# Kernel tuning notes

Hardware: AMD Instinct MI355X
Metric: run time of the kernel (lower is better)

## Reference

```python
import jax, jax.numpy as jnp
import numpy as np

N_HEAD = 16

def setup_inputs() -> dict:
    key = jax.random.key(0)
    k1, k2, k3, k4 = jax.random.split(key, 4)
    B, S, D = 4, 1024, 1024
    x = jax.random.normal(k1, (B, S, D), dtype=jnp.float32)
    # 0/1 float mask: cls_mask[:,0] overrides row 0, cls_mask[:,1] overrides col 0
    cls_mask = jax.random.randint(k2, (B, 2, S), 0, 2).astype(jnp.float32)
    w_attn = jax.random.normal(k3, (D, 3 * D), dtype=jnp.float32) * 0.02
    b_attn = jnp.zeros((3 * D,), dtype=jnp.float32)
    w_proj = jax.random.normal(k4, (D, D), dtype=jnp.float32) * 0.02
    b_proj = jnp.zeros((D,), dtype=jnp.float32)
    return {"x": x, "cls_mask": cls_mask, "w_attn": w_attn, "b_attn": b_attn,
            "w_proj": w_proj, "b_proj": b_proj}

def reference(x, cls_mask, w_attn, b_attn, w_proj, b_proj):
    B, S, D = x.shape
    H = N_HEAD
    hd = D // H
    cm = jnp.broadcast_to(jnp.tril(jnp.ones((S, S), x.dtype))[None, None], (B, 1, S, S))
    cm = cm.at[:, :, 0, :].set(cls_mask[:, 0][:, None, :])
    cm = cm.at[:, :, :, 0].set(cls_mask[:, 1][:, None, :])
    qkv = x @ w_attn + b_attn                      # [B,S,3D]
    q, k, v = jnp.split(qkv, 3, axis=-1)
    split_heads = lambda t: t.reshape(B, S, H, hd).transpose(0, 2, 1, 3)  # [B,H,S,hd]
    q, k, v = split_heads(q), split_heads(k), split_heads(v)
    w = jnp.einsum('bhqd,bhkd->bhqk', q, k) / jnp.sqrt(jnp.asarray(hd, x.dtype))
    w = w * cm - 10000.0 * (1.0 - cm)
    w = jax.nn.softmax(w, axis=-1)
    a = jnp.einsum('bhqk,bhkd->bhqd', w, v)
    a = a.transpose(0, 2, 1, 3).reshape(B, S, D)   # merge heads
    a = a @ w_proj + b_proj
    present = jnp.stack((k, v))                    # [2,B,H,S,hd]
    return a, present
```

## Files before the change

### kernel.cpp

```cpp
#include <hip/hip_runtime.h>
#include <hip/hip_bf16.h>

typedef __bf16 bf16x8 __attribute__((ext_vector_type(8)));
typedef float f32x4 __attribute__((ext_vector_type(4)));

__device__ __forceinline__ f32x4 mfma16(bf16x8 a, bf16x8 b, f32x4 c) {
    return __builtin_amdgcn_mfma_f32_16x16x32_bf16(a, b, c, 0, 0, 0);
}

typedef __attribute__((address_space(1))) const unsigned int GUInt;
typedef __attribute__((address_space(3))) unsigned int LUInt;
__device__ __forceinline__ void gl_lds16(const void* g, void* l) {
    __builtin_amdgcn_global_load_lds((GUInt*)g, (LUInt*)l, 16, 0, 0);
}

__device__ __forceinline__ int psw(int row, int bir) {
    return row * 128 + (bir ^ ((row & 7) << 4));
}

__global__ __launch_bounds__(256) void prep_kernel(
    const float* __restrict__ x, __hip_bfloat16* __restrict__ Xbf,
    const float* __restrict__ w_attn, __hip_bfloat16* __restrict__ WattnT,
    const float* __restrict__ w_proj, __hip_bfloat16* __restrict__ WprojT) {
    __shared__ float tile[64][65];
    const int bid = blockIdx.x;
    const int tid = threadIdx.x;
    if (bid < 4096) {
        int i = bid * 256 + tid;
        float4 v = reinterpret_cast<const float4*>(x)[i];
        __hip_bfloat16 o[4];
        o[0] = __float2bfloat16(v.x); o[1] = __float2bfloat16(v.y);
        o[2] = __float2bfloat16(v.z); o[3] = __float2bfloat16(v.w);
        *reinterpret_cast<uint2*>(&Xbf[i * 4]) = *reinterpret_cast<const uint2*>(o);
        return;
    }
    const float* in; __hip_bfloat16* out; int K, N, t;
    if (bid < 4096 + 768) { t = bid - 4096; in = w_attn; out = WattnT; K = 1024; N = 3072; }
    else                  { t = bid - 4864; in = w_proj; out = WprojT; K = 1024; N = 1024; }
    const int kt = t & 15, nt = t >> 4;
    const int c = tid & 63, r4 = tid >> 6;
#pragma unroll
    for (int i = 0; i < 16; ++i) {
        int r = i * 4 + r4;
        tile[r][c] = in[(size_t)(kt * 64 + r) * N + nt * 64 + c];
    }
    __syncthreads();
#pragma unroll
    for (int i = 0; i < 16; ++i) {
        int rr = i * 4 + r4;
        out[(size_t)(nt * 64 + rr) * K + kt * 64 + c] = __float2bfloat16(tile[c][rr]);
    }
}

template <int EPI>
__global__ __launch_bounds__(256) void gemm_kernel(
    const __hip_bfloat16* __restrict__ A, const __hip_bfloat16* __restrict__ Bt,
    const float* __restrict__ bias, int M, int N, int K,
    float* __restrict__ Cf,
    __hip_bfloat16* __restrict__ Qbf, __hip_bfloat16* __restrict__ Kbf,
    __hip_bfloat16* __restrict__ VbfT, float* __restrict__ present) {
    __shared__ __align__(16) char As[128 * 128];
    __shared__ __align__(16) char Bs[128 * 128];
    const int tid = threadIdx.x;
    const int lane = tid & 63;
    const int w = tid >> 6;
    const int lr = lane & 15;
    const int lg = lane >> 4;
    const int wm = (w >> 1) * 64;
    const int wn = (w & 1) * 64;
    const int bm = blockIdx.y, bn = blockIdx.x;
    const int swz = (lr & 7) << 4;

    const int srow = tid >> 3;
    const int ccs = ((tid & 7) * 16) ^ ((srow & 7) << 4);
    const char* aBase = (const char*)A + ((size_t)(bm * 128 + srow) * K) * 2 + ccs;
    const char* bBase = (const char*)Bt + ((size_t)(bn * 128 + srow) * K) * 2 + ccs;

    f32x4 zv = {0.f, 0.f, 0.f, 0.f};
    f32x4 acc[4][4];
#pragma unroll
    for (int i = 0; i < 4; ++i)
#pragma unroll
        for (int j = 0; j < 4; ++j) acc[i][j] = zv;

    for (int k0 = 0; k0 < K; k0 += 64) {
#pragma unroll
        for (int j = 0; j < 4; ++j) {
            gl_lds16(aBase + ((size_t)j * 32 * K + k0) * 2, &As[j * 4096 + tid * 16]);
            gl_lds16(bBase + ((size_t)j * 32 * K + k0) * 2, &Bs[j * 4096 + tid * 16]);
        }
        __syncthreads();
#pragma unroll
        for (int kk = 0; kk < 2; ++kk) {
            bf16x8 af[4], bfr[4];
#pragma unroll
            for (int mt = 0; mt < 4; ++mt)
                af[mt] = *reinterpret_cast<const bf16x8*>(
                    &As[(wm + mt * 16 + lr) * 128 + ((kk * 64 + lg * 16) ^ swz)]);
#pragma unroll
            for (int nt = 0; nt < 4; ++nt)
                bfr[nt] = *reinterpret_cast<const bf16x8*>(
                    &Bs[(wn + nt * 16 + lr) * 128 + ((kk * 64 + lg * 16) ^ swz)]);
#pragma unroll
            for (int mt = 0; mt < 4; ++mt)
#pragma unroll
                for (int nt = 0; nt < 4; ++nt)
                    acc[mt][nt] = mfma16(af[mt], bfr[nt], acc[mt][nt]);
        }
        __syncthreads();
    }

    const float SCQ = 0.18033688011112f;
#pragma unroll
    for (int mt = 0; mt < 4; ++mt) {
        const int mbase = bm * 128 + wm + mt * 16 + lg * 4;
        const int bb = mbase >> 10, s0 = mbase & 1023;
#pragma unroll
        for (int nt = 0; nt < 4; ++nt) {
            const int n = bn * 128 + wn + nt * 16 + lr;
            const float bias_n = bias[n];
            float v[4];
#pragma unroll
            for (int r = 0; r < 4; ++r) v[r] = acc[mt][nt][r] + bias_n;
            if (EPI == 0) {
#pragma unroll
                for (int r = 0; r < 4; ++r) Cf[(size_t)(mbase + r) * N + n] = v[r];
            } else {
                const int sec = n >> 10, nn = n & 1023;
                const int hh = nn >> 6, d = nn & 63;
                const int rowbase = ((bb * 16 + hh) * 1024 + s0) * 64 + d;
                if (sec == 0) {
#pragma unroll
                    for (int r = 0; r < 4; ++r)
                        Qbf[rowbase + r * 64] = __float2bfloat16(v[r] * SCQ);
                } else if (sec == 1) {
#pragma unroll
                    for (int r = 0; r < 4; ++r) {
                        Kbf[rowbase + r * 64] = __float2bfloat16(v[r]);
                        present[rowbase + r * 64] = v[r];
                    }
                } else {
                    __hip_bfloat16 pk[4];
#pragma unroll
                    for (int r = 0; r < 4; ++r) {
                        pk[r] = __float2bfloat16(v[r]);
                        present[4194304 + rowbase + r * 64] = v[r];
                    }
                    *reinterpret_cast<uint2*>(&VbfT[((bb * 16 + hh) * 64 + d) * 1024 + s0]) =
                        *reinterpret_cast<const uint2*>(pk);
                }
            }
        }
    }
}

template <bool FIRST>
__device__ __forceinline__ void attn_tile(
    const char* Kb, const char* Vb, int kv0, char* Pw,
    const bf16x8* aq, const float* clscol, const float* cls, int b, int qbase,
    f32x4* acc_o, f32x4& acc_l,
    int lr, int lg, int lk, int swz, bf16x8 ones) {
    f32x4 zv = {0.f, 0.f, 0.f, 0.f};
    f32x4 sacc[4];
#pragma unroll
    for (int nt = 0; nt < 4; ++nt) {
        const char* kr = Kb + (nt * 16 + lr) * 128;
        bf16x8 k0 = *reinterpret_cast<const bf16x8*>(kr + ((lg * 16) ^ swz));
        bf16x8 k1 = *reinterpret_cast<const bf16x8*>(kr + ((64 + lg * 16) ^ swz));
        sacc[nt] = mfma16(aq[1], k1, mfma16(aq[0], k0, zv));
    }
    float p[4][4];
#pragma unroll
    for (int nt = 0; nt < 4; ++nt) {
        int k_j = kv0 + nt * 16 + lr;
#pragma unroll
        for (int r = 0; r < 4; ++r) {
            int q_i = qbase + lg * 4 + r;
            float e = __builtin_amdgcn_exp2f(sacc[nt][r]);
            p[nt][r] = (k_j <= q_i) ? e : 0.f;
        }
    }
    if (qbase == 0) {
#pragma unroll
        for (int nt = 0; nt < 4; ++nt) {
            float cr = cls[b * 2048 + kv0 + nt * 16 + lr];
            float e0 = __builtin_amdgcn_exp2f(sacc[nt][0]);
            float pr = (cr != 0.f) ? e0 : 0.f;
            if (lg == 0) p[nt][0] = pr;
        }
    }
    if (FIRST) {
#pragma unroll
        for (int r = 0; r < 4; ++r) {
            float ec = __builtin_amdgcn_exp2f(sacc[0][r]);
            float pc = (clscol[r] != 0.f) ? ec : 0.f;
            if (lr == 0) p[0][r] = pc;
        }
    }
#pragma unroll
    for (int nt = 0; nt < 4; ++nt)
#pragma unroll
        for (int r = 0; r < 4; ++r)
            *reinterpret_cast<__hip_bfloat16*>(&Pw[psw(lg * 4 + r, nt * 32 + lr * 2)]) =
                __float2bfloat16(p[nt][r]);
    bf16x8 pa0 = *reinterpret_cast<const bf16x8*>(&Pw[psw(lr, lk * 2)]);
    bf16x8 pa1 = *reinterpret_cast<const bf16x8*>(&Pw[psw(lr, 64 + lk * 2)]);
    acc_l = mfma16(pa1, ones, mfma16(pa0, ones, acc_l));
#pragma unroll
    for (int ntd = 0; ntd < 4; ++ntd) {
        const char* vr = Vb + (ntd * 16 + lr) * 128;
        bf16x8 v0 = *reinterpret_cast<const bf16x8*>(vr + ((lg * 16) ^ swz));
        bf16x8 v1 = *reinterpret_cast<const bf16x8*>(vr + ((64 + lg * 16) ^ swz));
        acc_o[ntd] = mfma16(pa1, v1, mfma16(pa0, v0, acc_o[ntd]));
    }
}

__global__ __launch_bounds__(256) void attn_kernel(
    const __hip_bfloat16* __restrict__ Qbf, const __hip_bfloat16* __restrict__ Kbf,
    const __hip_bfloat16* __restrict__ VbfT, const float* __restrict__ cls,
    __hip_bfloat16* __restrict__ Abf) {
    __shared__ __align__(16) char KV0[16384];
    __shared__ __align__(16) char KV1[16384];
    __shared__ __align__(16) char P_lds[4 * 2048];
    const int tid = threadIdx.x;
    const int lane = tid & 63;
    const int w = tid >> 6;
    const int lr = lane & 15;
    const int lg = lane >> 4;
    const int lk = lg * 8;
    const int bh = blockIdx.x;
    const int qx = blockIdx.y;
    const int b = bh >> 4, h = bh & 15;
    const int qtmap[16] = {0, 15, 14, 10, 13, 12, 11, 9, 4, 6, 3, 8, 2, 1, 5, 7};
    const int qt = qtmap[qx];
    const int qbase = qt * 64 + w * 16;
    char* Pw = &P_lds[w * 2048];
    const int ntiles = (qt == 0) ? 16 : (qt + 1);

    const char* kSrc = (const char*)Kbf + (size_t)bh * 131072;
    const char* vSrc = (const char*)VbfT + (size_t)bh * 131072;
    const int srow = tid >> 3;
    const int ccs = ((tid & 7) * 16) ^ ((srow & 7) << 4);

#define STAGE(BUFPTR, T)                                                         \
    do {                                                                         \
        const int kv0s_ = (T) * 64;                                              \
        char* dst_ = &(BUFPTR)[tid * 16];                                        \
        gl_lds16(kSrc + (size_t)(kv0s_ + srow) * 128 + ccs, dst_);               \
        gl_lds16(kSrc + (size_t)(kv0s_ + 32 + srow) * 128 + ccs, dst_ + 4096);   \
        gl_lds16(vSrc + (size_t)srow * 2048 + kv0s_ * 2 + ccs, dst_ + 8192);     \
        gl_lds16(vSrc + (size_t)(32 + srow) * 2048 + kv0s_ * 2 + ccs, dst_ + 12288); \
    } while (0)

    STAGE(KV0, 0);

    bf16x8 aq[2];
#pragma unroll
    for (int c = 0; c < 2; ++c)
        aq[c] = *reinterpret_cast<const bf16x8*>(&Qbf[(size_t)(bh * 1024 + qbase + lr) * 64 + c * 32 + lk]);

    float clscol[4];
#pragma unroll
    for (int r = 0; r < 4; ++r)
        clscol[r] = cls[b * 2048 + 1024 + qbase + lg * 4 + r];

    bf16x8 ones;
#pragma unroll
    for (int i = 0; i < 8; ++i) ones[i] = (__bf16)1.0f;

    f32x4 zv = {0.f, 0.f, 0.f, 0.f};
    f32x4 acc_o[4];
    f32x4 acc_l = zv;
#pragma unroll
    for (int i = 0; i < 4; ++i) acc_o[i] = zv;

    const int swz = (lr & 7) << 4;
    __syncthreads();

    STAGE(KV1, 1);
    attn_tile<true>(KV0, KV0 + 8192, 0, Pw, aq, clscol, cls, b, qbase,
                    acc_o, acc_l, lr, lg, lk, swz, ones);
    __syncthreads();
    int t = 1;
    while (t < ntiles) {
        if (t + 1 < ntiles) STAGE(KV0, t + 1);
        attn_tile<false>(KV1, KV1 + 8192, t * 64, Pw, aq, clscol, cls, b, qbase,
                         acc_o, acc_l, lr, lg, lk, swz, ones);
        __syncthreads();
        ++t;
        if (t >= ntiles) break;
        if (t + 1 < ntiles) STAGE(KV1, t + 1);
        attn_tile<false>(KV0, KV0 + 8192, t * 64, Pw, aq, clscol, cls, b, qbase,
                         acc_o, acc_l, lr, lg, lk, swz, ones);
        __syncthreads();
        ++t;
    }
#undef STAGE

#pragma unroll
    for (int r = 0; r < 4; ++r) {
        float inv = 1.f / acc_l[r];
        int q_i = qbase + lg * 4 + r;
#pragma unroll
        for (int ntd = 0; ntd < 4; ++ntd) {
            int dd = ntd * 16 + lr;
            Abf[(size_t)(b * 1024 + q_i) * 1024 + h * 64 + dd] = __float2bfloat16(acc_o[ntd][r] * inv);
        }
    }
}

extern "C" void kernel_launch(void* const* d_in, const int* in_sizes, int n_in,
                              void* d_out, int out_size, void* d_ws, size_t ws_size,
                              hipStream_t stream) {
    const float* x      = (const float*)d_in[0];
    const float* cls    = (const float*)d_in[1];
    const float* w_attn = (const float*)d_in[2];
    const float* b_attn = (const float*)d_in[3];
    const float* w_proj = (const float*)d_in[4];
    const float* b_proj = (const float*)d_in[5];
    float* out_a = (float*)d_out;
    float* present = out_a + 4194304;

    char* ws = (char*)d_ws;
    __hip_bfloat16* Xbf    = (__hip_bfloat16*)(ws);
    __hip_bfloat16* Abf    = (__hip_bfloat16*)(ws);
    __hip_bfloat16* WattnT = (__hip_bfloat16*)(ws + 12ull * 1024 * 1024);
    __hip_bfloat16* WprojT = (__hip_bfloat16*)(ws + 20ull * 1024 * 1024);
    __hip_bfloat16* Qbf    = (__hip_bfloat16*)(ws + 24ull * 1024 * 1024);
    __hip_bfloat16* Kbf    = (__hip_bfloat16*)(ws + 36ull * 1024 * 1024);
    __hip_bfloat16* VbfT   = (__hip_bfloat16*)(ws + 48ull * 1024 * 1024);

    prep_kernel<<<5120, 256, 0, stream>>>(x, Xbf, w_attn, WattnT, w_proj, WprojT);
    gemm_kernel<1><<<dim3(24, 32), 256, 0, stream>>>(Xbf, WattnT, b_attn, 4096, 3072, 1024,
                                                     nullptr, Qbf, Kbf, VbfT, present);
    attn_kernel<<<dim3(64, 16), 256, 0, stream>>>(Qbf, Kbf, VbfT, cls, Abf);
    gemm_kernel<0><<<dim3(8, 32), 256, 0, stream>>>(Abf, WprojT, b_proj, 4096, 1024, 1024,
                                                    out_a, nullptr, nullptr, nullptr, nullptr);
}
```

Measured before the change: 104.9 us.

## Use 256x256 double-buffered 512-thread GEMM kernel for QKV projection

Replaces the 128x128 single-buffered QKV GEMM with a 256x256-tile, 512-thread kernel. It double-buffers LDS via global_load_lds with explicit vmcnt waits and barriers, and raises wave priority around the MFMA bursts. Larger tiles raise data reuse per LDS load, and the double buffering overlaps global loads with compute. The trade-off is fewer blocks (192 on a 256-CU device, so some CUs sit idle), 128KB of LDS per block, and heavier register pressure from the 8x4 accumulator array.

```diff
diff --git a/kernel.cpp b/kernel.cpp
--- a/kernel.cpp
+++ b/kernel.cpp
@@ -52,13 +52,144 @@
     }
 }
 
+#define VW8() asm volatile("s_waitcnt vmcnt(8)" ::: "memory")
+#define VW0() asm volatile("s_waitcnt vmcnt(0)" ::: "memory")
+#define BAR() do { __builtin_amdgcn_sched_barrier(0); __builtin_amdgcn_s_barrier(); \
+                   __builtin_amdgcn_sched_barrier(0); } while (0)
+
+__global__ __launch_bounds__(512) void gemm256_kernel(
+    const __hip_bfloat16* __restrict__ A, const __hip_bfloat16* __restrict__ Bt,
+    const float* __restrict__ bias,
+    __hip_bfloat16* __restrict__ Qbf, __hip_bfloat16* __restrict__ Kbf,
+    __hip_bfloat16* __restrict__ VbfT, float* __restrict__ present) {
+    constexpr int K = 1024;
+    __shared__ __align__(16) char As[2][32768];
+    __shared__ __align__(16) char Bs[2][32768];
+    const int tid = threadIdx.x;
+    const int lane = tid & 63;
+    const int w = tid >> 6;
+    const int lr = lane & 15;
+    const int lg = lane >> 4;
+    const int wm = (w >> 2) * 128;
+    const int wn = (w & 3) * 64;
+    const int bm = blockIdx.y, bn = blockIdx.x;
+    const int swz = (lr & 7) << 4;
+
+    const int srow = tid >> 3;
+    const int ccs = ((tid & 7) * 16) ^ ((srow & 7) << 4);
+    const char* aBase = (const char*)A + ((size_t)(bm * 256 + srow) * K) * 2 + ccs;
+    const char* bBase = (const char*)Bt + ((size_t)(bn * 256 + srow) * K) * 2 + ccs;
+
+#define STAGE256(BUF, KT)                                                        \
+    do {                                                                         \
+        const size_t koff_ = (size_t)(KT) * 128;                                 \
+        _Pragma("unroll")                                                        \
+        for (int j_ = 0; j_ < 4; ++j_) {                                         \
+            gl_lds16(aBase + (size_t)j_ * 64 * 2048 + koff_,                     \
+                     &As[BUF][j_ * 8192 + tid * 16]);                            \
+            gl_lds16(bBase + (size_t)j_ * 64 * 2048 + koff_,                     \
+                     &Bs[BUF][j_ * 8192 + tid * 16]);                            \
+        }                                                                        \
+    } while (0)
+
+    f32x4 zv = {0.f, 0.f, 0.f, 0.f};
+    f32x4 acc[8][4];
+#pragma unroll
+    for (int i = 0; i < 8; ++i)
+#pragma unroll
+        for (int j = 0; j < 4; ++j) acc[i][j] = zv;
+
+#define COMPUTE256(B)                                                            \
+    do {                                                                         \
+        bf16x8 bfr_[4][2];                                                       \
+        _Pragma("unroll")                                                        \
+        for (int nf = 0; nf < 4; ++nf)                                           \
+            _Pragma("unroll")                                                    \
+            for (int ks = 0; ks < 2; ++ks)                                       \
+                bfr_[nf][ks] = *reinterpret_cast<const bf16x8*>(                 \
+                    &Bs[B][(wn + nf * 16 + lr) * 128 + ((ks * 64 + lg * 16) ^ swz)]); \
+        _Pragma("unroll")                                                        \
+        for (int mh = 0; mh < 2; ++mh) {                                         \
+            bf16x8 af_[4][2];                                                    \
+            _Pragma("unroll")                                                    \
+            for (int mf = 0; mf < 4; ++mf)                                       \
+                _Pragma("unroll")                                                \
+                for (int ks = 0; ks < 2; ++ks)                                   \
+                    af_[mf][ks] = *reinterpret_cast<const bf16x8*>(              \
+                        &As[B][(wm + (mh * 4 + mf) * 16 + lr) * 128 +            \
+                               ((ks * 64 + lg * 16) ^ swz)]);                    \
+            __builtin_amdgcn_s_setprio(1);                                       \
+            _Pragma("unroll")                                                    \
+            for (int mf = 0; mf < 4; ++mf)                                       \
+                _Pragma("unroll")                                                \
+                for (int nf = 0; nf < 4; ++nf) {                                 \
+                    acc[mh * 4 + mf][nf] =                                       \
+                        mfma16(af_[mf][0], bfr_[nf][0], acc[mh * 4 + mf][nf]);   \
+                    acc[mh * 4 + mf][nf] =                                       \
+                        mfma16(af_[mf][1], bfr_[nf][1], acc[mh * 4 + mf][nf]);   \
+                }                                                                \
+            __builtin_amdgcn_s_setprio(0);                                       \
+        }                                                                        \
+    } while (0)
+
+    STAGE256(0, 0);
+    for (int kt = 0; kt < 16; kt += 2) {
+        if (kt + 1 < 16) { STAGE256(1, kt + 1); VW8(); } else { VW0(); }
+        BAR();
+        COMPUTE256(0);
+        BAR();
+        if (kt + 2 < 16) { STAGE256(0, kt + 2); VW8(); } else { VW0(); }
+        BAR();
+        COMPUTE256(1);
+        BAR();
+    }
+#undef STAGE256
+#undef COMPUTE256
+
+    const float SCQ = 0.18033688011112f;
+#pragma unroll
+    for (int mt = 0; mt < 8; ++mt) {
+        const int mbase = bm * 256 + wm + mt * 16 + lg * 4;
+        const int bb = mbase >> 10, s0 = mbase & 1023;
+#pragma unroll
+        for (int nt = 0; nt < 4; ++nt) {
+            const int n = bn * 256 + wn + nt * 16 + lr;
+            const float bias_n = bias[n];
+            float v[4];
+#pragma unroll
+            for (int r = 0; r < 4; ++r) v[r] = acc[mt][nt][r] + bias_n;
+            const int sec = n >> 10, nn = n & 1023;
+            const int hh = nn >> 6, d = nn & 63;
+            const int rowbase = ((bb * 16 + hh) * 1024 + s0) * 64 + d;
+            if (sec == 0) {
+#pragma unroll
+                for (int r = 0; r < 4; ++r)
+                    Qbf[rowbase + r * 64] = __float2bfloat16(v[r] * SCQ);
+            } else if (sec == 1) {
+#pragma unroll
+                for (int r = 0; r < 4; ++r) {
+                    Kbf[rowbase + r * 64] = __float2bfloat16(v[r]);
+                    present[rowbase + r * 64] = v[r];
+                }
+            } else {
+                __hip_bfloat16 pk[4];
+#pragma unroll
+                for (int r = 0; r < 4; ++r) {
+                    pk[r] = __float2bfloat16(v[r]);
+                    present[4194304 + rowbase + r * 64] = v[r];
+                }
+                *reinterpret_cast<uint2*>(&VbfT[((bb * 16 + hh) * 64 + d) * 1024 + s0]) =
+                    *reinterpret_cast<const uint2*>(pk);
+            }
+        }
+    }
+}
+
 template <int EPI>
 __global__ __launch_bounds__(256) void gemm_kernel(
     const __hip_bfloat16* __restrict__ A, const __hip_bfloat16* __restrict__ Bt,
     const float* __restrict__ bias, int M, int N, int K,
-    float* __restrict__ Cf,
-    __hip_bfloat16* __restrict__ Qbf, __hip_bfloat16* __restrict__ Kbf,
-    __hip_bfloat16* __restrict__ VbfT, float* __restrict__ present) {
+    float* __restrict__ Cf) {
     __shared__ __align__(16) char As[128 * 128];
     __shared__ __align__(16) char Bs[128 * 128];
     const int tid = threadIdx.x;
@@ -110,46 +241,16 @@
         __syncthreads();
     }
 
-    const float SCQ = 0.18033688011112f;
 #pragma unroll
     for (int mt = 0; mt < 4; ++mt) {
         const int mbase = bm * 128 + wm + mt * 16 + lg * 4;
-        const int bb = mbase >> 10, s0 = mbase & 1023;
 #pragma unroll
         for (int nt = 0; nt < 4; ++nt) {
             const int n = bn * 128 + wn + nt * 16 + lr;
             const float bias_n = bias[n];
-            float v[4];
-#pragma unroll
-            for (int r = 0; r < 4; ++r) v[r] = acc[mt][nt][r] + bias_n;
-            if (EPI == 0) {
-#pragma unroll
-                for (int r = 0; r < 4; ++r) Cf[(size_t)(mbase + r) * N + n] = v[r];
-            } else {
-                const int sec = n >> 10, nn = n & 1023;
-                const int hh = nn >> 6, d = nn & 63;
-                const int rowbase = ((bb * 16 + hh) * 1024 + s0) * 64 + d;
-                if (sec == 0) {
-#pragma unroll
-                    for (int r = 0; r < 4; ++r)
-                        Qbf[rowbase + r * 64] = __float2bfloat16(v[r] * SCQ);
-                } else if (sec == 1) {
-#pragma unroll
-                    for (int r = 0; r < 4; ++r) {
-                        Kbf[rowbase + r * 64] = __float2bfloat16(v[r]);
-                        present[rowbase + r * 64] = v[r];
-                    }
-                } else {
-                    __hip_bfloat16 pk[4];
-#pragma unroll
-                    for (int r = 0; r < 4; ++r) {
-                        pk[r] = __float2bfloat16(v[r]);
-                        present[4194304 + rowbase + r * 64] = v[r];
-                    }
-                    *reinterpret_cast<uint2*>(&VbfT[((bb * 16 + hh) * 64 + d) * 1024 + s0]) =
-                        *reinterpret_cast<const uint2*>(pk);
-                }
-            }
+#pragma unroll
+            for (int r = 0; r < 4; ++r)
+                Cf[(size_t)(mbase + r) * N + n] = acc[mt][nt][r] + bias_n;
         }
     }
 }
@@ -331,9 +432,9 @@
     __hip_bfloat16* VbfT   = (__hip_bfloat16*)(ws + 48ull * 1024 * 1024);
 
     prep_kernel<<<5120, 256, 0, stream>>>(x, Xbf, w_attn, WattnT, w_proj, WprojT);
-    gemm_kernel<1><<<dim3(24, 32), 256, 0, stream>>>(Xbf, WattnT, b_attn, 4096, 3072, 1024,
-                                                     nullptr, Qbf, Kbf, VbfT, present);
+    gemm256_kernel<<<dim3(12, 16), 512, 0, stream>>>(Xbf, WattnT, b_attn,
+                                                     Qbf, Kbf, VbfT, present);
     attn_kernel<<<dim3(64, 16), 256, 0, stream>>>(Qbf, Kbf, VbfT, cls, Abf);
     gemm_kernel<0><<<dim3(8, 32), 256, 0, stream>>>(Abf, WprojT, b_proj, 4096, 1024, 1024,
-                                                    out_a, nullptr, nullptr, nullptr, nullptr);
-}
+                                                    out_a);
+}
```

After: 107.2 us. 2.2% more time.
